# Optimization experiments

Hardware: AMD Instinct MI355X
Metric: run time of the kernel (lower is better)

The kernel has to match this reference:

```python
import jax, jax.numpy as jnp
import numpy as np

D_MODEL = 1024
N_HEADS = 16
HEAD_DIM = D_MODEL // N_HEADS
N_EXPERTS = 4
HIDDEN = 4 * D_MODEL
B, T = 1, 2048


def _apply_rope(x, sin, cos):
    # x: [..., D]; sin/cos broadcastable to [..., D/2]
    x1, x2 = x[..., ::2], x[..., 1::2]
    r1 = x1 * cos - x2 * sin
    r2 = x1 * sin + x2 * cos
    return jnp.stack((r1, r2), axis=-1).reshape(x.shape)


def setup_inputs() -> dict:
    key = jax.random.key(0)
    ks = jax.random.split(key, 16)
    s = 0.02
    d, E, Hd = D_MODEL, N_EXPERTS, HIDDEN
    return {
        "x": jax.random.normal(ks[0], (B, T, d), dtype=jnp.float32),
        "w_dw": jax.random.normal(ks[1], (d, 3), dtype=jnp.float32) * s,      # depthwise conv k=3
        "w_pw": jax.random.normal(ks[2], (d, d), dtype=jnp.float32) * s,      # pointwise conv [out,in]
        "w_qkv": jax.random.normal(ks[3], (3 * d, d), dtype=jnp.float32) * s,  # [out,in]
        "w_o": jax.random.normal(ks[4], (d, d), dtype=jnp.float32) * s,
        "w_gate": jax.random.normal(ks[5], (d, d), dtype=jnp.float32) * s,
        "b_gate": jnp.zeros((d,), dtype=jnp.float32),
        "ln_g": jnp.ones((d,), dtype=jnp.float32),
        "ln_b": jnp.zeros((d,), dtype=jnp.float32),
        "w_moe_gate": jax.random.normal(ks[6], (E, d), dtype=jnp.float32) * s,  # Linear no bias [out,in]
        "w1": jax.random.normal(ks[7], (E, Hd, d), dtype=jnp.float32) * s,
        "b1": jnp.zeros((E, Hd), dtype=jnp.float32),
        "w2": jax.random.normal(ks[8], (E, d, Hd), dtype=jnp.float32) * s,
        "b2": jnp.zeros((E, d), dtype=jnp.float32),
    }


def reference(x, w_dw, w_pw, w_qkv, w_o, w_gate, b_gate, ln_g, ln_b,
              w_moe_gate, w1, b1, w2, b2):
    Bv, Tv, d = x.shape
    H, Dh = N_HEADS, HEAD_DIM
    dt = x.dtype

    # --- causal conv mixer (depthwise k=3, causal left pad 2, then pointwise) ---
    xp = jnp.pad(x, ((0, 0), (2, 0), (0, 0)))
    y = (xp[:, 0:Tv] * w_dw[:, 0] + xp[:, 1:Tv + 1] * w_dw[:, 1]
         + xp[:, 2:Tv + 2] * w_dw[:, 2])
    y = jnp.einsum('btd,ed->bte', y, w_pw)
    x = x + y

    # --- qkv projection + split heads ---
    qkv = jnp.einsum('btd,ed->bte', x, w_qkv).reshape(Bv, Tv, 3, H, Dh)
    q, k, v = qkv[:, :, 0], qkv[:, :, 1], qkv[:, :, 2]

    # --- RoPE (head_dim even) ---
    inv_freq = 1.0 / (10000.0 ** (jnp.arange(0, Dh, 2, dtype=dt) / Dh))
    pos = jnp.arange(Tv, dtype=dt)
    theta = pos[:, None] * inv_freq[None, :]                 # [T, Dh/2]
    sin = jnp.sin(theta)[None, :, None, :]                   # [1,T,1,Dh/2]
    cos = jnp.cos(theta)[None, :, None, :]
    q = _apply_rope(q, sin, cos)
    k = _apply_rope(k, sin, cos)

    # --- linear attention via full kv outer-product cumsum ---
    q_phi = jax.nn.elu(q) + 1.0
    k_phi = jax.nn.elu(k) + 1.0
    kv = k_phi[..., :, None] * v[..., None, :]               # [B,T,H,D,D]
    kv_prefix = jnp.cumsum(kv, axis=1)
    k_prefix = jnp.cumsum(k_phi, axis=1)
    num = jnp.einsum('bthd,bthdm->bthm', q_phi, kv_prefix)
    denom = jnp.sum(q_phi * k_prefix, axis=-1, keepdims=True)
    attn = num / (denom + 1e-6)
    attn = attn.reshape(Bv, Tv, d)
    attn = jnp.einsum('btd,ed->bte', attn, w_o)

    # --- delta-gated residual (dropout = identity in eval) ---
    delta = x - jnp.concatenate([x[:, :1], x[:, :-1]], axis=1)
    gate = jax.nn.sigmoid(jnp.einsum('btd,ed->bte', delta, w_gate) + b_gate)
    x = x + gate * attn

    # --- LayerNorm + dense MoE FFN ---
    mu = jnp.mean(x, axis=-1, keepdims=True)
    var = jnp.mean((x - mu) ** 2, axis=-1, keepdims=True)
    h = (x - mu) / jnp.sqrt(var + 1e-5) * ln_g + ln_b

    gw = jax.nn.softmax(jnp.einsum('btd,ed->bte', h, w_moe_gate), axis=-1)  # [B,T,E]
    hid = jax.nn.silu(jnp.einsum('btd,efd->btef', h, w1) + b1)              # [B,T,E,Hd]
    eo = jnp.einsum('btef,edf->bted', hid, w2) + b2                          # [B,T,E,d]
    ffn = jnp.einsum('bte,bted->btd', gw, eo)
    return x + ffn
```

## Files before the change

### kernel.cpp

```cpp
#include <hip/hip_runtime.h>
#include <hip/hip_bf16.h>

#define TSEQ 2048
#define DM   1024
#define NHD  16
#define DHD  64
#define NEXP 4
#define HIDN 4096
#define NMOE (NEXP*HIDN)
#define CHK  128
#define NCHK (TSEQ/CHK)

typedef __attribute__((ext_vector_type(8))) short          bf16x8_v;
typedef __attribute__((ext_vector_type(4))) float          f32x4_v;
typedef __attribute__((ext_vector_type(4))) unsigned short us4_v;

__device__ __forceinline__ unsigned short bfbits(float f) {
  __hip_bfloat16 h = __float2bfloat16(f);
  return __builtin_bit_cast(unsigned short, h);
}
__device__ __forceinline__ float bf2f(unsigned short u) {
  return __uint_as_float(((unsigned)u) << 16);
}
__device__ __forceinline__ float wave_sum(float v) {
  #pragma unroll
  for (int o = 32; o; o >>= 1) v += __shfl_xor(v, o, 64);
  return v;
}
__device__ __forceinline__ void gl_lds16(const void* g, void* l) {
  __builtin_amdgcn_global_load_lds((const __attribute__((address_space(1))) void*)g,
                                   (__attribute__((address_space(3))) void*)l, 16, 0, 0);
}

__global__ __launch_bounds__(256) void cvt_bf16(const float* __restrict__ in,
                                                unsigned short* __restrict__ out, int n4) {
  int i = blockIdx.x * 256 + threadIdx.x;
  if (i >= n4) return;
  float4 v = ((const float4*)in)[i];
  us4_v o; o.x = bfbits(v.x); o.y = bfbits(v.y); o.z = bfbits(v.z); o.w = bfbits(v.w);
  ((us4_v*)out)[i] = o;
}

__global__ __launch_bounds__(256) void perm_w2(const float* __restrict__ in,
                                               unsigned short* __restrict__ out) {
  int i = blockIdx.x * 256 + threadIdx.x;
  int i4 = i * 4;
  int f = i4 & (HIDN - 1);
  int r = i4 >> 12;
  int e = r >> 10, dd = r & 1023;
  float4 v = *(const float4*)&in[(size_t)r * HIDN + f];
  us4_v o; o.x = bfbits(v.x); o.y = bfbits(v.y); o.z = bfbits(v.z); o.w = bfbits(v.w);
  *(us4_v*)&out[(size_t)dd * NMOE + e * HIDN + f] = o;
}

__global__ __launch_bounds__(256) void conv_dw(const float* __restrict__ x,
                                               const float* __restrict__ w_dw,
                                               unsigned short* __restrict__ y_bf) {
  int i = blockIdx.x * 256 + threadIdx.x;
  int c = i & (DM - 1);
  int t = i >> 10;
  float a = (t >= 2) ? x[i - 2 * DM] : 0.f;
  float b = (t >= 1) ? x[i - DM]     : 0.f;
  float d = x[i];
  float y = a * w_dw[c * 3] + b * w_dw[c * 3 + 1] + d * w_dw[c * 3 + 2];
  y_bf[i] = bfbits(y);
}

template <int EPI>
__global__ __launch_bounds__(256) void gemm_bt(
    const unsigned short* __restrict__ A,  const unsigned short* __restrict__ A2,
    const unsigned short* __restrict__ B,  const unsigned short* __restrict__ B2,
    float* __restrict__ Cf, float* __restrict__ Cf2,
    unsigned short* __restrict__ Cbf,
    const float* __restrict__ ex0,
    int lda, int ldb, int K, int ldc)
{
  if (EPI == 0) { if (blockIdx.z) { A = A2; B = B2; Cf = Cf2; } }

  __shared__ unsigned short As[2][128][32];
  __shared__ unsigned short Bs[2][128][32];

  const int tid = threadIdx.x;
  const int m0 = blockIdx.x << 7, n0 = blockIdx.y << 7;
  const int sr = tid >> 2, sc = (tid & 3) << 3;
  const unsigned short* gA = A + (size_t)(m0 + sr) * lda + sc;
  const unsigned short* gB = B + (size_t)(n0 + sr) * ldb + sc;

  const int lane = tid & 63, wv = tid >> 6;
  const int wr = (wv >> 1) << 6, wc = (wv & 1) << 6;
  const int fr = lane & 15, fk = (lane >> 4) << 3, r4 = (lane >> 4) << 2;

  f32x4_v acc[4][4] = {};

  auto stage = [&](int k0, int b) {
    gl_lds16(gA + k0,                     &As[b][sr][sc]);
    gl_lds16(gA + k0 + (size_t)64 * lda,  &As[b][sr + 64][sc]);
    gl_lds16(gB + k0,                     &Bs[b][sr][sc]);
    gl_lds16(gB + k0 + (size_t)64 * ldb,  &Bs[b][sr + 64][sc]);
  };

  stage(0, 0);
  __syncthreads();
  int cur = 0;
  for (int k0 = 0; k0 < K; k0 += 32) {
    if (k0 + 32 < K) stage(k0 + 32, cur ^ 1);
    bf16x8_v af[4], bfm[4];
    #pragma unroll
    for (int m = 0; m < 4; m++) af[m]  = *(const bf16x8_v*)&As[cur][wr + m * 16 + fr][fk];
    #pragma unroll
    for (int n = 0; n < 4; n++) bfm[n] = *(const bf16x8_v*)&Bs[cur][wc + n * 16 + fr][fk];
    #pragma unroll
    for (int m = 0; m < 4; m++)
      #pragma unroll
      for (int n = 0; n < 4; n++)
        acc[m][n] = __builtin_amdgcn_mfma_f32_16x16x32_bf16(af[m], bfm[n], acc[m][n], 0, 0, 0);
    __syncthreads();
    cur ^= 1;
  }

  #pragma unroll
  for (int m = 0; m < 4; m++) {
    #pragma unroll
    for (int n = 0; n < 4; n++) {
      #pragma unroll
      for (int j = 0; j < 4; j++) {
        int gr = m0 + wr + m * 16 + r4 + j;
        int gc = n0 + wc + n * 16 + fr;
        float v = acc[m][n][j];
        size_t off = (size_t)gr * ldc + gc;
        if (EPI == 0) {
          Cf[off] = v;
        } else {
          float s = v + ex0[off];
          Cf[off] = s; Cbf[off] = bfbits(s);
        }
      }
    }
  }
}

template <int EPI>
__global__ __launch_bounds__(512, 1) void gemm256(
    const unsigned short* __restrict__ A, const unsigned short* __restrict__ B,
    float* __restrict__ Cf, unsigned short* __restrict__ Cbf,
    const float* __restrict__ ex0, const float* __restrict__ ex1,
    int lda, int ldb, int K, int ldc, int kPerZ)
{
  if (EPI == 1) { int ko = blockIdx.z * kPerZ; A += ko; B += ko; K = kPerZ; }

  __shared__ unsigned short As[2][256][64];
  __shared__ unsigned short Bs[2][256][64];

  int bidl = blockIdx.y * 8 + blockIdx.x;
  int chunk = (gridDim.x * gridDim.y) >> 3;
  int swz = (bidl & 7) * chunk + (bidl >> 3);
  int m0 = (swz & 7) << 8, n0 = (swz >> 3) << 8;

  const int tid = threadIdx.x;
  const int srow = tid >> 3;
  const int scol = (tid & 7) << 3;
  const int scsw = scol ^ (((tid >> 5) & 1) << 4);
  const unsigned short* gA = A + (size_t)(m0 + srow) * lda + scsw;
  const unsigned short* gB = B + (size_t)(n0 + srow) * ldb + scsw;

  auto stage = [&](int k0, int b) {
    #pragma unroll
    for (int i = 0; i < 4; i++)
      gl_lds16(gA + (size_t)(i * 64) * lda + k0, &As[b][i * 64 + srow][scol]);
    #pragma unroll
    for (int i = 0; i < 4; i++)
      gl_lds16(gB + (size_t)(i * 64) * ldb + k0, &Bs[b][i * 64 + srow][scol]);
  };

  const int lane = tid & 63, wv = tid >> 6;
  const int wm = wv >> 2, wn = wv & 3;
  const int fr = lane & 15;
  const int fksw = ((lane >> 4) << 3) ^ (((fr >> 2) & 1) << 4);
  const int r4 = (lane >> 4) << 2;

  f32x4_v acc[8][4] = {};
  stage(0, 0);
  int cur = 0;
  for (int k0 = 0; k0 < K; k0 += 64) {
    if (k0 + 64 < K) {
      stage(k0 + 64, cur ^ 1);
      asm volatile("s_waitcnt vmcnt(8)" ::: "memory");
    } else {
      asm volatile("s_waitcnt vmcnt(0)" ::: "memory");
    }
    __builtin_amdgcn_s_barrier();
    __builtin_amdgcn_sched_barrier(0);
    #pragma unroll
    for (int ks = 0; ks < 2; ks++) {
      bf16x8_v a[8], bb[4];
      #pragma unroll
      for (int m = 0; m < 8; m++)
        a[m] = *(const bf16x8_v*)&As[cur][wm * 128 + m * 16 + fr][ks * 32 + fksw];
      #pragma unroll
      for (int n = 0; n < 4; n++)
        bb[n] = *(const bf16x8_v*)&Bs[cur][wn * 64 + n * 16 + fr][ks * 32 + fksw];
      #pragma unroll
      for (int m = 0; m < 8; m++)
        #pragma unroll
        for (int n = 0; n < 4; n++)
          acc[m][n] = __builtin_amdgcn_mfma_f32_16x16x32_bf16(a[m], bb[n], acc[m][n], 0, 0, 0);
    }
    __builtin_amdgcn_sched_barrier(0);
    __builtin_amdgcn_s_barrier();
    cur ^= 1;
  }

  #pragma unroll
  for (int m = 0; m < 8; m++)
    #pragma unroll
    for (int n = 0; n < 4; n++)
      #pragma unroll
      for (int j = 0; j < 4; j++) {
        int grow = m0 + wm * 128 + m * 16 + r4 + j;
        int gcol = n0 + wn * 64 + n * 16 + fr;
        size_t off = (size_t)grow * ldc + gcol;
        if (EPI == 0) {
          float c2 = acc[m][n][j] + ex0[gcol];
          float sl = c2 / (1.f + __expf(-c2));
          Cbf[off] = bfbits(sl * ex1[grow * 4 + (gcol >> 12)]);
        } else {
          atomicAdd(&Cf[off], acc[m][n][j]);
        }
      }
}

__global__ __launch_bounds__(256) void rope_phi(const float* __restrict__ qkv,
                                                unsigned short* __restrict__ qphi,
                                                unsigned short* __restrict__ kphi,
                                                unsigned short* __restrict__ vout) {
  int idx = blockIdx.x * 256 + threadIdx.x;
  int i = idx & 31;
  int h = (idx >> 5) & 15;
  int t = idx >> 9;
  const float* row = qkv + (size_t)t * 3 * DM;
  int col = h * 64 + 2 * i;
  float q0 = row[col],          q1 = row[col + 1];
  float k0 = row[DM + col],     k1 = row[DM + col + 1];
  float v0 = row[2 * DM + col], v1 = row[2 * DM + col + 1];
  float invf = __expf(-(float)(2 * i) * (9.210340371976184f / 64.f));
  float th = (float)t * invf;
  float s, c;
  sincosf(th, &s, &c);
  float qr0 = q0 * c - q1 * s, qr1 = q0 * s + q1 * c;
  float kr0 = k0 * c - k1 * s, kr1 = k0 * s + k1 * c;
  size_t o = (size_t)t * DM + col;
  qphi[o]     = bfbits(qr0 > 0.f ? qr0 + 1.f : __expf(qr0));
  qphi[o + 1] = bfbits(qr1 > 0.f ? qr1 + 1.f : __expf(qr1));
  kphi[o]     = bfbits(kr0 > 0.f ? kr0 + 1.f : __expf(kr0));
  kphi[o + 1] = bfbits(kr1 > 0.f ? kr1 + 1.f : __expf(kr1));
  vout[o]     = bfbits(v0);
  vout[o + 1] = bfbits(v1);
}

__global__ __launch_bounds__(256) void kv_chunk(const unsigned short* __restrict__ kphi,
                                                const unsigned short* __restrict__ vbf,
                                                float* __restrict__ kvT,
                                                float* __restrict__ ksbuf) {
  int h = blockIdx.x & 15, c = blockIdx.x >> 4;
  __shared__ unsigned short Kt[64][136];
  __shared__ unsigned short Vt[64][136];
  int tid = threadIdx.x;
  int rr = tid >> 3, cc = (tid & 7) << 3;
  int t0 = c * CHK;
  #pragma unroll
  for (int g = 0; g < 4; g++) {
    int t = g * 32 + rr;
    bf16x8_v k8 = *(const bf16x8_v*)&kphi[(size_t)(t0 + t) * DM + h * 64 + cc];
    bf16x8_v v8 = *(const bf16x8_v*)&vbf [(size_t)(t0 + t) * DM + h * 64 + cc];
    #pragma unroll
    for (int j = 0; j < 8; j++) { Kt[cc + j][t] = (unsigned short)k8[j];
                                  Vt[cc + j][t] = (unsigned short)v8[j]; }
  }
  __syncthreads();
  int lane = tid & 63, wv = tid >> 6;
  int wr = (wv >> 1) << 5, wc = (wv & 1) << 5;
  int fr = lane & 15, fk = (lane >> 4) << 3, r4 = (lane >> 4) << 2;
  f32x4_v acc[2][2] = {};
  #pragma unroll
  for (int k0 = 0; k0 < 128; k0 += 32) {
    bf16x8_v a[2], b[2];
    #pragma unroll
    for (int m = 0; m < 2; m++) a[m] = *(const bf16x8_v*)&Kt[wr + m * 16 + fr][k0 + fk];
    #pragma unroll
    for (int n = 0; n < 2; n++) b[n] = *(const bf16x8_v*)&Vt[wc + n * 16 + fr][k0 + fk];
    #pragma unroll
    for (int m = 0; m < 2; m++)
      #pragma unroll
      for (int n = 0; n < 2; n++)
        acc[m][n] = __builtin_amdgcn_mfma_f32_16x16x32_bf16(a[m], b[n], acc[m][n], 0, 0, 0);
  }
  float* kvout = kvT + (size_t)(h * NCHK + c) * 4096;
  #pragma unroll
  for (int m = 0; m < 2; m++)
    #pragma unroll
    for (int n = 0; n < 2; n++)
      #pragma unroll
      for (int j = 0; j < 4; j++)
        kvout[(wc + n * 16 + fr) * 64 + (wr + m * 16 + r4 + j)] = acc[m][n][j];
  float s = 0.f;
  int d = tid >> 2, q = tid & 3;
  for (int i = 0; i < 32; i++) s += bf2f(Kt[d][q * 32 + i]);
  s += __shfl_xor(s, 1, 64); s += __shfl_xor(s, 2, 64);
  if (q == 0) ksbuf[(h * NCHK + c) * 64 + d] = s;
}

__global__ __launch_bounds__(256) void prefix_kv(const float* __restrict__ kvT,
                                                 const float* __restrict__ ksbuf,
                                                 unsigned short* __restrict__ sT,
                                                 float* __restrict__ kspre) {
  int idx = blockIdx.x * 256 + threadIdx.x;
  int h = idx >> 12, nd = idx & 4095;
  float s = 0.f;
  for (int c = 0; c < NCHK; c++) {
    size_t o = (size_t)(h * NCHK + c) * 4096 + nd;
    sT[o] = bfbits(s);
    s += kvT[o];
  }
  if (idx < NHD * 64) {
    float ks = 0.f;
    for (int c = 0; c < NCHK; c++) {
      int o = ((idx >> 6) * NCHK + c) * 64 + (idx & 63);
      kspre[o] = ks;
      ks += ksbuf[o];
    }
  }
}

__global__ __launch_bounds__(256) void attn_chunk(const unsigned short* __restrict__ qphi,
                                                  const unsigned short* __restrict__ kphi,
                                                  const unsigned short* __restrict__ vbf,
                                                  const unsigned short* __restrict__ sT,
                                                  const float* __restrict__ kspre,
                                                  float* __restrict__ num,
                                                  float* __restrict__ den) {
  int h = blockIdx.x & 15, c = blockIdx.x >> 4;
  __shared__ unsigned short Qs[128][72];
  __shared__ unsigned short Ks[128][72];
  __shared__ unsigned short Ms[128][200];
  __shared__ unsigned short Vt[64][200];
  __shared__ float ksL[64];
  int tid = threadIdx.x;
  int t0 = c * CHK;
  int rr = tid >> 3, cc = (tid & 7) << 3;
  #pragma unroll
  for (int g = 0; g < 4; g++) {
    int t = g * 32 + rr;
    bf16x8_v q8 = *(const bf16x8_v*)&qphi[(size_t)(t0 + t) * DM + h * 64 + cc];
    bf16x8_v k8 = *(const bf16x8_v*)&kphi[(size_t)(t0 + t) * DM + h * 64 + cc];
    bf16x8_v v8 = *(const bf16x8_v*)&vbf [(size_t)(t0 + t) * DM + h * 64 + cc];
    *(bf16x8_v*)&Qs[t][cc] = q8;
    *(bf16x8_v*)&Ks[t][cc] = k8;
    *(bf16x8_v*)&Ms[t][128 + cc] = q8;
    #pragma unroll
    for (int j = 0; j < 8; j++) Vt[cc + j][t] = (unsigned short)v8[j];
  }
  #pragma unroll
  for (int g = 0; g < 2; g++) {
    int e = (g * 256 + tid) * 8;
    bf16x8_v s8 = *(const bf16x8_v*)&sT[(size_t)(h * NCHK + c) * 4096 + e];
    *(bf16x8_v*)&Vt[e >> 6][128 + (e & 63)] = s8;
  }
  if (tid < 64) ksL[tid] = kspre[(h * NCHK + c) * 64 + tid];
  __syncthreads();

  int lane = tid & 63, wv = tid >> 6;
  int wr = (wv >> 1) << 6, wc = (wv & 1) << 6;
  int fr = lane & 15, fk = (lane >> 4) << 3, r4 = (lane >> 4) << 2;
  {
    f32x4_v acc[4][4] = {};
    #pragma unroll
    for (int k0 = 0; k0 < 64; k0 += 32) {
      bf16x8_v a[4], b[4];
      #pragma unroll
      for (int m = 0; m < 4; m++) a[m] = *(const bf16x8_v*)&Qs[wr + m * 16 + fr][k0 + fk];
      #pragma unroll
      for (int n = 0; n < 4; n++) b[n] = *(const bf16x8_v*)&Ks[wc + n * 16 + fr][k0 + fk];
      #pragma unroll
      for (int m = 0; m < 4; m++)
        #pragma unroll
        for (int n = 0; n < 4; n++)
          acc[m][n] = __builtin_amdgcn_mfma_f32_16x16x32_bf16(a[m], b[n], acc[m][n], 0, 0, 0);
    }
    #pragma unroll
    for (int m = 0; m < 4; m++)
      #pragma unroll
      for (int n = 0; n < 4; n++)
        #pragma unroll
        for (int j = 0; j < 4; j++) {
          int r = wr + m * 16 + r4 + j, col = wc + n * 16 + fr;
          Ms[r][col] = bfbits(col <= r ? acc[m][n][j] : 0.f);
        }
  }
  __syncthreads();
  {
    int dr = tid >> 1, half = tid & 1;
    float s = 0.f;
    for (int i = 0; i < 64; i++) s += bf2f(Ms[dr][half * 64 + i]);
    for (int i = 0; i < 32; i++) {
      int d = half * 32 + i;
      s += bf2f(Qs[dr][d]) * ksL[d];
    }
    s += __shfl_xor(s, 1, 64);
    if (!half) den[(size_t)(t0 + dr) * NHD + h] = s;
  }
  {
    int wc2 = (wv & 1) << 5;
    f32x4_v acc[4][2] = {};
    #pragma unroll
    for (int k0 = 0; k0 < 192; k0 += 32) {
      bf16x8_v a[4], b[2];
      #pragma unroll
      for (int m = 0; m < 4; m++) a[m] = *(const bf16x8_v*)&Ms[wr + m * 16 + fr][k0 + fk];
      #pragma unroll
      for (int n = 0; n < 2; n++) b[n] = *(const bf16x8_v*)&Vt[wc2 + n * 16 + fr][k0 + fk];
      #pragma unroll
      for (int m = 0; m < 4; m++)
        #pragma unroll
        for (int n = 0; n < 2; n++)
          acc[m][n] = __builtin_amdgcn_mfma_f32_16x16x32_bf16(a[m], b[n], acc[m][n], 0, 0, 0);
    }
    #pragma unroll
    for (int m = 0; m < 4; m++)
      #pragma unroll
      for (int n = 0; n < 2; n++)
        #pragma unroll
        for (int j = 0; j < 4; j++)
          num[(size_t)(t0 + wr + m * 16 + r4 + j) * DM + h * 64 + wc2 + n * 16 + fr]
              = acc[m][n][j];
  }
}

__global__ __launch_bounds__(256) void div_cvt(const float* __restrict__ attn_num,
                                               const float* __restrict__ denom,
                                               const float* __restrict__ x1,
                                               unsigned short* __restrict__ attn_bf,
                                               unsigned short* __restrict__ delta_bf) {
  int i = blockIdx.x * 256 + threadIdx.x;
  int i4 = i * 4;
  int t = i4 >> 10, c = i4 & 1023, h = c >> 6;
  float dn = 1.f / (denom[t * NHD + h] + 1e-6f);
  float4 nm = *(const float4*)&attn_num[i4];
  us4_v a; a.x = bfbits(nm.x * dn); a.y = bfbits(nm.y * dn);
           a.z = bfbits(nm.z * dn); a.w = bfbits(nm.w * dn);
  *(us4_v*)&attn_bf[i4] = a;
  float4 xv = *(const float4*)&x1[i4];
  float4 xp = t ? *(const float4*)&x1[i4 - DM] : xv;
  us4_v d; d.x = bfbits(xv.x - xp.x); d.y = bfbits(xv.y - xp.y);
           d.z = bfbits(xv.z - xp.z); d.w = bfbits(xv.w - xp.w);
  *(us4_v*)&delta_bf[i4] = d;
}

__global__ __launch_bounds__(256) void fuse_ln(const float* __restrict__ x1,
                                               const float* __restrict__ attn_o,
                                               const float* __restrict__ gate_lin,
                                               const float* __restrict__ b_gate,
                                               const float* __restrict__ ln_g,
                                               const float* __restrict__ ln_b,
                                               const float* __restrict__ w_moe,
                                               float* __restrict__ x2,
                                               unsigned short* __restrict__ h_bf,
                                               float* __restrict__ gw) {
  int t = blockIdx.x;
  int tid = threadIdx.x;
  __shared__ float hrow[DM];
  __shared__ float red[16];
  float vals[4], s = 0.f, s2 = 0.f;
  #pragma unroll
  for (int j = 0; j < 4; j++) {
    int c = tid + j * 256;
    size_t ix = (size_t)t * DM + c;
    float g = gate_lin[ix] + b_gate[c];
    float sig = 1.f / (1.f + __expf(-g));
    float xv = x1[ix] + sig * attn_o[ix];
    x2[ix] = xv; vals[j] = xv; s += xv; s2 += xv * xv;
  }
  s = wave_sum(s); s2 = wave_sum(s2);
  int wvi = tid >> 6, l = tid & 63;
  if (l == 0) { red[wvi] = s; red[4 + wvi] = s2; }
  __syncthreads();
  s  = red[0] + red[1] + red[2] + red[3];
  s2 = red[4] + red[5] + red[6] + red[7];
  float mu = s * (1.f / DM);
  float var = s2 * (1.f / DM) - mu * mu;
  float rstd = rsqrtf(var + 1e-5f);
  #pragma unroll
  for (int j = 0; j < 4; j++) {
    int c = tid + j * 256;
    size_t ix = (size_t)t * DM + c;
    float h = (vals[j] - mu) * rstd * ln_g[c] + ln_b[c];
    h_bf[ix] = bfbits(h); hrow[c] = h;
  }
  __syncthreads();
  float dot = 0.f;
  for (int i0 = l; i0 < DM; i0 += 64) dot += hrow[i0] * w_moe[wvi * DM + i0];
  dot = wave_sum(dot);
  if (l == 0) red[8 + wvi] = dot;
  __syncthreads();
  if (tid == 0) {
    float a0 = red[8], a1 = red[9], a2 = red[10], a3 = red[11];
    float mx = fmaxf(fmaxf(a0, a1), fmaxf(a2, a3));
    float e0 = __expf(a0 - mx), e1 = __expf(a1 - mx), e2 = __expf(a2 - mx), e3 = __expf(a3 - mx);
    float inv = 1.f / (e0 + e1 + e2 + e3);
    gw[t * 4 + 0] = e0 * inv; gw[t * 4 + 1] = e1 * inv;
    gw[t * 4 + 2] = e2 * inv; gw[t * 4 + 3] = e3 * inv;
  }
}

__global__ __launch_bounds__(256) void init_out(const float* __restrict__ x2,
                                                const float* __restrict__ gw,
                                                const float* __restrict__ b2,
                                                float* __restrict__ out) {
  int i = blockIdx.x * 256 + threadIdx.x;
  int i4 = i * 4;
  int t = i4 >> 10, c = i4 & 1023;
  const float* g = gw + t * 4;
  float4 o = *(const float4*)&x2[i4];
  #pragma unroll
  for (int e = 0; e < 4; e++) {
    float ge = g[e];
    float4 b = *(const float4*)&b2[e * DM + c];
    o.x += ge * b.x; o.y += ge * b.y; o.z += ge * b.z; o.w += ge * b.w;
  }
  *(float4*)&out[i4] = o;
}

extern "C" void kernel_launch(void* const* d_in, const int* in_sizes, int n_in,
                              void* d_out, int out_size, void* d_ws, size_t ws_size,
                              hipStream_t stream) {
  const float* x      = (const float*)d_in[0];
  const float* w_dw   = (const float*)d_in[1];
  const float* w_pw   = (const float*)d_in[2];
  const float* w_qkv  = (const float*)d_in[3];
  const float* w_o    = (const float*)d_in[4];
  const float* w_gate = (const float*)d_in[5];
  const float* b_gate = (const float*)d_in[6];
  const float* ln_g   = (const float*)d_in[7];
  const float* ln_b   = (const float*)d_in[8];
  const float* w_moe  = (const float*)d_in[9];
  const float* w1     = (const float*)d_in[10];
  const float* b1     = (const float*)d_in[11];
  const float* w2     = (const float*)d_in[12];
  const float* b2     = (const float*)d_in[13];
  float* out = (float*)d_out;

  char* ws = (char*)d_ws;
  size_t off = 0;
  auto alloc = [&](size_t bytes) -> char* {
    char* p = ws + off; off += (bytes + 255) & ~(size_t)255; return p;
  };
  unsigned short* w_pw_bf   = (unsigned short*)alloc((size_t)DM * DM * 2);
  unsigned short* w_qkv_bf  = (unsigned short*)alloc((size_t)3 * DM * DM * 2);
  unsigned short* w_o_bf    = (unsigned short*)alloc((size_t)DM * DM * 2);
  unsigned short* w_gate_bf = (unsigned short*)alloc((size_t)DM * DM * 2);
  unsigned short* w1_bf     = (unsigned short*)alloc((size_t)NMOE * DM * 2);
  unsigned short* w2c_bf    = (unsigned short*)alloc((size_t)DM * NMOE * 2);
  float*          x1        = (float*)alloc((size_t)TSEQ * DM * 4);
  unsigned short* x1_bf     = (unsigned short*)alloc((size_t)TSEQ * DM * 2);
  unsigned short* y_bf      = (unsigned short*)alloc((size_t)TSEQ * DM * 2);
  float*          denomb    = (float*)alloc((size_t)TSEQ * NHD * 4);
  float*          gwb       = (float*)alloc((size_t)TSEQ * NEXP * 4);
  float*          attn_o    = (float*)alloc((size_t)TSEQ * DM * 4);
  unsigned short* delta_bf  = (unsigned short*)alloc((size_t)TSEQ * DM * 2);
  float*          gate_lin  = (float*)alloc((size_t)TSEQ * DM * 4);
  float*          x2        = (float*)alloc((size_t)TSEQ * DM * 4);
  unsigned short* h_bf      = (unsigned short*)alloc((size_t)TSEQ * DM * 2);
  float*          kvT       = (float*)alloc((size_t)NHD * NCHK * 4096 * 4);
  unsigned short* sTb       = (unsigned short*)alloc((size_t)NHD * NCHK * 4096 * 2);
  float*          ksbuf     = (float*)alloc((size_t)NHD * NCHK * 64 * 4);
  float*          kspre     = (float*)alloc((size_t)NHD * NCHK * 64 * 4);
  char*           pool      = alloc((size_t)TSEQ * NMOE * 2);
  if (off > ws_size) return;

  float*          qkv      = (float*)pool;
  unsigned short* qphi     = (unsigned short*)(pool + (size_t)TSEQ * 3 * DM * 4);
  unsigned short* kphi     = qphi + (size_t)TSEQ * DM;
  unsigned short* vbf      = kphi + (size_t)TSEQ * DM;
  float*          attn_num = (float*)(vbf + (size_t)TSEQ * DM);
  unsigned short* attn_bf  = (unsigned short*)(attn_num + (size_t)TSEQ * DM);
  unsigned short* hids     = (unsigned short*)pool;

  cvt_bf16<<<1024,  256, 0, stream>>>(w_pw,   w_pw_bf,   DM * DM / 4);
  cvt_bf16<<<3072,  256, 0, stream>>>(w_qkv,  w_qkv_bf,  3 * DM * DM / 4);
  cvt_bf16<<<1024,  256, 0, stream>>>(w_o,    w_o_bf,    DM * DM / 4);
  cvt_bf16<<<1024,  256, 0, stream>>>(w_gate, w_gate_bf, DM * DM / 4);
  cvt_bf16<<<16384, 256, 0, stream>>>(w1,     w1_bf,     NMOE * DM / 4);
  perm_w2<<<16384, 256, 0, stream>>>(w2, w2c_bf);

  conv_dw<<<8192, 256, 0, stream>>>(x, w_dw, y_bf);
  gemm_bt<1><<<dim3(16, 8, 1), 256, 0, stream>>>(y_bf, nullptr, w_pw_bf, nullptr,
      x1, nullptr, x1_bf, x, DM, DM, DM, DM);

  gemm_bt<0><<<dim3(16, 24, 1), 256, 0, stream>>>(x1_bf, nullptr, w_qkv_bf, nullptr,
      qkv, nullptr, nullptr, nullptr, DM, DM, DM, 3 * DM);
  rope_phi<<<4096, 256, 0, stream>>>(qkv, qphi, kphi, vbf);

  kv_chunk<<<NHD * NCHK, 256, 0, stream>>>(kphi, vbf, kvT, ksbuf);
  prefix_kv<<<256, 256, 0, stream>>>(kvT, ksbuf, sTb, kspre);
  attn_chunk<<<NHD * NCHK, 256, 0, stream>>>(qphi, kphi, vbf, sTb, kspre,
                                             attn_num, denomb);
  div_cvt<<<2048, 256, 0, stream>>>(attn_num, denomb, x1, attn_bf, delta_bf);

  gemm_bt<0><<<dim3(16, 8, 2), 256, 0, stream>>>(attn_bf, delta_bf, w_o_bf, w_gate_bf,
      attn_o, gate_lin, nullptr, nullptr, DM, DM, DM, DM);

  fuse_ln<<<2048, 256, 0, stream>>>(x1, attn_o, gate_lin, b_gate, ln_g, ln_b, w_moe,
                                    x2, h_bf, gwb);

  init_out<<<2048, 256, 0, stream>>>(x2, gwb, b2, out);
  gemm256<0><<<dim3(8, 64, 1), 512, 0, stream>>>(h_bf, w1_bf, nullptr, hids,
      b1, gwb, DM, DM, DM, NMOE, 0);
  gemm256<1><<<dim3(8, 4, 8), 512, 0, stream>>>(hids, w2c_bf, out, nullptr,
      nullptr, nullptr, NMOE, NMOE, NMOE, DM, NMOE / 8);
}
```

Baseline: 418.1 us.

## Restructure gemm256 main loop into quadrant-interleaved MFMA phases with split A/B staging

Splits each K-tile of the 256x256 GEMM into four sub-phases: fragments for one quadrant are loaded from LDS while MFMAs run on another, with wave priority raised around the MFMA bursts. The next tile's A and B global-to-LDS loads are issued at different points in the loop, and the LDS swizzle becomes a full 3-bit XOR pattern. The block-index linearisation now uses gridDim.x instead of a hard-coded 8. The aim is to hide LDS read latency and bank conflicts behind matrix work. The cost is extra barriers per tile and a different register pressure profile.

```diff
diff --git a/kernel.cpp b/kernel.cpp
--- a/kernel.cpp
+++ b/kernel.cpp
@@ -151,7 +151,7 @@
   __shared__ unsigned short As[2][256][64];
   __shared__ unsigned short Bs[2][256][64];
 
-  int bidl = blockIdx.y * 8 + blockIdx.x;
+  int bidl = blockIdx.y * gridDim.x + blockIdx.x;
   int chunk = (gridDim.x * gridDim.y) >> 3;
   int swz = (bidl & 7) * chunk + (bidl >> 3);
   int m0 = (swz & 7) << 8, n0 = (swz >> 3) << 8;
@@ -159,14 +159,16 @@
   const int tid = threadIdx.x;
   const int srow = tid >> 3;
   const int scol = (tid & 7) << 3;
-  const int scsw = scol ^ (((tid >> 5) & 1) << 4);
+  const int scsw = (((tid & 7) ^ ((tid >> 3) & 7)) << 3);
   const unsigned short* gA = A + (size_t)(m0 + srow) * lda + scsw;
   const unsigned short* gB = B + (size_t)(n0 + srow) * ldb + scsw;
 
-  auto stage = [&](int k0, int b) {
+  auto stageA = [&](int k0, int b) {
     #pragma unroll
     for (int i = 0; i < 4; i++)
       gl_lds16(gA + (size_t)(i * 64) * lda + k0, &As[b][i * 64 + srow][scol]);
+  };
+  auto stageB = [&](int k0, int b) {
     #pragma unroll
     for (int i = 0; i < 4; i++)
       gl_lds16(gB + (size_t)(i * 64) * ldb + k0, &Bs[b][i * 64 + srow][scol]);
@@ -175,39 +177,85 @@
   const int lane = tid & 63, wv = tid >> 6;
   const int wm = wv >> 2, wn = wv & 3;
   const int fr = lane & 15;
-  const int fksw = ((lane >> 4) << 3) ^ (((fr >> 2) & 1) << 4);
-  const int r4 = (lane >> 4) << 2;
+  const int kreg = lane >> 4, r4 = kreg << 2;
+  const int c0 = ((kreg) ^ (lane & 7)) << 3;
+  const int c1 = ((4 + kreg) ^ (lane & 7)) << 3;
 
   f32x4_v acc[8][4] = {};
-  stage(0, 0);
-  int cur = 0;
-  for (int k0 = 0; k0 < K; k0 += 64) {
-    if (k0 + 64 < K) {
-      stage(k0 + 64, cur ^ 1);
-      asm volatile("s_waitcnt vmcnt(8)" ::: "memory");
+  bf16x8_v a0[4][2], a1[4][2], bb[2][2];
+
+  stageA(0, 0); stageB(0, 0);
+  const int nt = K >> 6;
+  for (int t = 0; t < nt; t++) {
+    const int p = t & 1;
+    if (t + 1 < nt) {
+      stageA((t + 1) << 6, p ^ 1);
+      asm volatile("s_waitcnt vmcnt(4)" ::: "memory");
     } else {
       asm volatile("s_waitcnt vmcnt(0)" ::: "memory");
     }
     __builtin_amdgcn_s_barrier();
-    __builtin_amdgcn_sched_barrier(0);
-    #pragma unroll
-    for (int ks = 0; ks < 2; ks++) {
-      bf16x8_v a[8], bb[4];
-      #pragma unroll
-      for (int m = 0; m < 8; m++)
-        a[m] = *(const bf16x8_v*)&As[cur][wm * 128 + m * 16 + fr][ks * 32 + fksw];
-      #pragma unroll
-      for (int n = 0; n < 4; n++)
-        bb[n] = *(const bf16x8_v*)&Bs[cur][wn * 64 + n * 16 + fr][ks * 32 + fksw];
-      #pragma unroll
-      for (int m = 0; m < 8; m++)
-        #pragma unroll
-        for (int n = 0; n < 4; n++)
-          acc[m][n] = __builtin_amdgcn_mfma_f32_16x16x32_bf16(a[m], bb[n], acc[m][n], 0, 0, 0);
-    }
-    __builtin_amdgcn_sched_barrier(0);
+    #pragma unroll
+    for (int m = 0; m < 4; m++) {
+      a0[m][0] = *(const bf16x8_v*)&As[p][wm * 128 + m * 16 + fr][c0];
+      a0[m][1] = *(const bf16x8_v*)&As[p][wm * 128 + m * 16 + fr][c1];
+    }
+    #pragma unroll
+    for (int n = 0; n < 2; n++) {
+      bb[n][0] = *(const bf16x8_v*)&Bs[p][wn * 64 + n * 16 + fr][c0];
+      bb[n][1] = *(const bf16x8_v*)&Bs[p][wn * 64 + n * 16 + fr][c1];
+    }
+    __builtin_amdgcn_s_setprio(1);
+    #pragma unroll
+    for (int m = 0; m < 4; m++)
+      #pragma unroll
+      for (int n = 0; n < 2; n++) {
+        acc[m][n] = __builtin_amdgcn_mfma_f32_16x16x32_bf16(a0[m][0], bb[n][0], acc[m][n], 0, 0, 0);
+        acc[m][n] = __builtin_amdgcn_mfma_f32_16x16x32_bf16(a0[m][1], bb[n][1], acc[m][n], 0, 0, 0);
+      }
+    __builtin_amdgcn_s_setprio(0);
     __builtin_amdgcn_s_barrier();
-    cur ^= 1;
+    #pragma unroll
+    for (int m = 0; m < 4; m++) {
+      a1[m][0] = *(const bf16x8_v*)&As[p][wm * 128 + 64 + m * 16 + fr][c0];
+      a1[m][1] = *(const bf16x8_v*)&As[p][wm * 128 + 64 + m * 16 + fr][c1];
+    }
+    __builtin_amdgcn_s_setprio(1);
+    #pragma unroll
+    for (int m = 0; m < 4; m++)
+      #pragma unroll
+      for (int n = 0; n < 2; n++) {
+        acc[m + 4][n] = __builtin_amdgcn_mfma_f32_16x16x32_bf16(a1[m][0], bb[n][0], acc[m + 4][n], 0, 0, 0);
+        acc[m + 4][n] = __builtin_amdgcn_mfma_f32_16x16x32_bf16(a1[m][1], bb[n][1], acc[m + 4][n], 0, 0, 0);
+      }
+    __builtin_amdgcn_s_setprio(0);
+    __builtin_amdgcn_s_barrier();
+    #pragma unroll
+    for (int n = 0; n < 2; n++) {
+      bb[n][0] = *(const bf16x8_v*)&Bs[p][wn * 64 + 32 + n * 16 + fr][c0];
+      bb[n][1] = *(const bf16x8_v*)&Bs[p][wn * 64 + 32 + n * 16 + fr][c1];
+    }
+    if (t + 1 < nt) stageB((t + 1) << 6, p ^ 1);
+    __builtin_amdgcn_s_setprio(1);
+    #pragma unroll
+    for (int m = 0; m < 4; m++)
+      #pragma unroll
+      for (int n = 0; n < 2; n++) {
+        acc[m][n + 2] = __builtin_amdgcn_mfma_f32_16x16x32_bf16(a0[m][0], bb[n][0], acc[m][n + 2], 0, 0, 0);
+        acc[m][n + 2] = __builtin_amdgcn_mfma_f32_16x16x32_bf16(a0[m][1], bb[n][1], acc[m][n + 2], 0, 0, 0);
+      }
+    __builtin_amdgcn_s_setprio(0);
+    __builtin_amdgcn_s_barrier();
+    __builtin_amdgcn_s_setprio(1);
+    #pragma unroll
+    for (int m = 0; m < 4; m++)
+      #pragma unroll
+      for (int n = 0; n < 2; n++) {
+        acc[m + 4][n + 2] = __builtin_amdgcn_mfma_f32_16x16x32_bf16(a1[m][0], bb[n][0], acc[m + 4][n + 2], 0, 0, 0);
+        acc[m + 4][n + 2] = __builtin_amdgcn_mfma_f32_16x16x32_bf16(a1[m][1], bb[n][1], acc[m + 4][n + 2], 0, 0, 0);
+      }
+    __builtin_amdgcn_s_setprio(0);
+    __builtin_amdgcn_s_barrier();
   }
 
   #pragma unroll
```

New measurement: 387.9 us. -7.2%, faster.

## Replace 256x256 MoE GEMM tiles with 128x128 tiles at two blocks per CU

Applied to the files above, without the earlier changes.

The MoE FFN GEMMs move from 256x256 tiles with 512 threads and one block per CU to 128x128 tiles with 256 threads and two blocks per CU. The LDS swizzle becomes a full 8-way XOR, and the workgroup-to-tile mapping is generalised. MFMA sections are raised to higher wave priority with s_setprio. The aim is more concurrent waves and better latency hiding, at the cost of lower per-tile data reuse and more global loads. For the split-K w2 GEMM it also means more atomic-add traffic.

```diff
diff --git a/kernel.cpp b/kernel.cpp
--- a/kernel.cpp
+++ b/kernel.cpp
@@ -140,7 +140,7 @@
 }
 
 template <int EPI>
-__global__ __launch_bounds__(512, 1) void gemm256(
+__global__ __launch_bounds__(256, 2) void gemm128(
     const unsigned short* __restrict__ A, const unsigned short* __restrict__ B,
     float* __restrict__ Cf, unsigned short* __restrict__ Cbf,
     const float* __restrict__ ex0, const float* __restrict__ ex1,
@@ -148,76 +148,85 @@
 {
   if (EPI == 1) { int ko = blockIdx.z * kPerZ; A += ko; B += ko; K = kPerZ; }
 
-  __shared__ unsigned short As[2][256][64];
-  __shared__ unsigned short Bs[2][256][64];
-
-  int bidl = blockIdx.y * 8 + blockIdx.x;
-  int chunk = (gridDim.x * gridDim.y) >> 3;
-  int swz = (bidl & 7) * chunk + (bidl >> 3);
-  int m0 = (swz & 7) << 8, n0 = (swz >> 3) << 8;
+  __shared__ unsigned short As[2][128][64];
+  __shared__ unsigned short Bs[2][128][64];
+
+  const int nwg = gridDim.x * gridDim.y;
+  const int bidl = blockIdx.y * gridDim.x + blockIdx.x;
+  const int chunk = nwg >> 3;
+  const int swz = (bidl & 7) * chunk + (bidl >> 3);
+  const int ntn = gridDim.y;
+  const int rest = swz >> 3;
+  const int m0 = ((rest / ntn) * 8 + (swz & 7)) << 7;
+  const int n0 = (rest % ntn) << 7;
 
   const int tid = threadIdx.x;
   const int srow = tid >> 3;
   const int scol = (tid & 7) << 3;
-  const int scsw = scol ^ (((tid >> 5) & 1) << 4);
+  const int scsw = (((tid & 7) ^ ((tid >> 3) & 7)) << 3);
   const unsigned short* gA = A + (size_t)(m0 + srow) * lda + scsw;
   const unsigned short* gB = B + (size_t)(n0 + srow) * ldb + scsw;
 
   auto stage = [&](int k0, int b) {
     #pragma unroll
     for (int i = 0; i < 4; i++)
-      gl_lds16(gA + (size_t)(i * 64) * lda + k0, &As[b][i * 64 + srow][scol]);
+      gl_lds16(gA + (size_t)(i * 32) * lda + k0, &As[b][i * 32 + srow][scol]);
     #pragma unroll
     for (int i = 0; i < 4; i++)
-      gl_lds16(gB + (size_t)(i * 64) * ldb + k0, &Bs[b][i * 64 + srow][scol]);
+      gl_lds16(gB + (size_t)(i * 32) * ldb + k0, &Bs[b][i * 32 + srow][scol]);
   };
 
   const int lane = tid & 63, wv = tid >> 6;
-  const int wm = wv >> 2, wn = wv & 3;
-  const int fr = lane & 15;
-  const int fksw = ((lane >> 4) << 3) ^ (((fr >> 2) & 1) << 4);
-  const int r4 = (lane >> 4) << 2;
-
-  f32x4_v acc[8][4] = {};
+  const int wr = (wv >> 1) << 6, wc = (wv & 1) << 6;
+  const int fr = lane & 15, kreg = lane >> 4, r4 = kreg << 2;
+  const int c0 = ((kreg) ^ (lane & 7)) << 3;
+  const int c1 = ((4 + kreg) ^ (lane & 7)) << 3;
+
+  f32x4_v acc[4][4] = {};
+
   stage(0, 0);
-  int cur = 0;
-  for (int k0 = 0; k0 < K; k0 += 64) {
-    if (k0 + 64 < K) {
-      stage(k0 + 64, cur ^ 1);
+  const int nt = K >> 6;
+  for (int t = 0; t < nt; t++) {
+    const int p = t & 1;
+    if (t + 1 < nt) {
+      stage((t + 1) << 6, p ^ 1);
       asm volatile("s_waitcnt vmcnt(8)" ::: "memory");
     } else {
       asm volatile("s_waitcnt vmcnt(0)" ::: "memory");
     }
     __builtin_amdgcn_s_barrier();
     __builtin_amdgcn_sched_barrier(0);
-    #pragma unroll
-    for (int ks = 0; ks < 2; ks++) {
-      bf16x8_v a[8], bb[4];
-      #pragma unroll
-      for (int m = 0; m < 8; m++)
-        a[m] = *(const bf16x8_v*)&As[cur][wm * 128 + m * 16 + fr][ks * 32 + fksw];
-      #pragma unroll
-      for (int n = 0; n < 4; n++)
-        bb[n] = *(const bf16x8_v*)&Bs[cur][wn * 64 + n * 16 + fr][ks * 32 + fksw];
-      #pragma unroll
-      for (int m = 0; m < 8; m++)
-        #pragma unroll
-        for (int n = 0; n < 4; n++)
-          acc[m][n] = __builtin_amdgcn_mfma_f32_16x16x32_bf16(a[m], bb[n], acc[m][n], 0, 0, 0);
-    }
-    __builtin_amdgcn_sched_barrier(0);
+    bf16x8_v af[4][2], bfm[4][2];
+    #pragma unroll
+    for (int m = 0; m < 4; m++) {
+      af[m][0] = *(const bf16x8_v*)&As[p][wr + m * 16 + fr][c0];
+      af[m][1] = *(const bf16x8_v*)&As[p][wr + m * 16 + fr][c1];
+    }
+    #pragma unroll
+    for (int n = 0; n < 4; n++) {
+      bfm[n][0] = *(const bf16x8_v*)&Bs[p][wc + n * 16 + fr][c0];
+      bfm[n][1] = *(const bf16x8_v*)&Bs[p][wc + n * 16 + fr][c1];
+    }
+    __builtin_amdgcn_s_setprio(1);
+    #pragma unroll
+    for (int m = 0; m < 4; m++)
+      #pragma unroll
+      for (int n = 0; n < 4; n++) {
+        acc[m][n] = __builtin_amdgcn_mfma_f32_16x16x32_bf16(af[m][0], bfm[n][0], acc[m][n], 0, 0, 0);
+        acc[m][n] = __builtin_amdgcn_mfma_f32_16x16x32_bf16(af[m][1], bfm[n][1], acc[m][n], 0, 0, 0);
+      }
+    __builtin_amdgcn_s_setprio(0);
     __builtin_amdgcn_s_barrier();
-    cur ^= 1;
-  }
-
-  #pragma unroll
-  for (int m = 0; m < 8; m++)
+  }
+
+  #pragma unroll
+  for (int m = 0; m < 4; m++)
     #pragma unroll
     for (int n = 0; n < 4; n++)
       #pragma unroll
       for (int j = 0; j < 4; j++) {
-        int grow = m0 + wm * 128 + m * 16 + r4 + j;
-        int gcol = n0 + wn * 64 + n * 16 + fr;
+        int grow = m0 + wr + m * 16 + r4 + j;
+        int gcol = n0 + wc + n * 16 + fr;
         size_t off = (size_t)grow * ldc + gcol;
         if (EPI == 0) {
           float c2 = acc[m][n][j] + ex0[gcol];
@@ -612,8 +621,8 @@
                                     x2, h_bf, gwb);
 
   init_out<<<2048, 256, 0, stream>>>(x2, gwb, b2, out);
-  gemm256<0><<<dim3(8, 64, 1), 512, 0, stream>>>(h_bf, w1_bf, nullptr, hids,
+  gemm128<0><<<dim3(16, 128, 1), 256, 0, stream>>>(h_bf, w1_bf, nullptr, hids,
       b1, gwb, DM, DM, DM, NMOE, 0);
-  gemm256<1><<<dim3(8, 4, 8), 512, 0, stream>>>(hids, w2c_bf, out, nullptr,
+  gemm128<1><<<dim3(16, 8, 8), 256, 0, stream>>>(hids, w2c_bf, out, nullptr,
       nullptr, nullptr, NMOE, NMOE, NMOE, DM, NMOE / 8);
 }
```

New measurement: 403.0 us. 3.6% less time.
